# Kernel tuning notes

Hardware: AMD Instinct MI355X
Metric: run time of the kernel (lower is better)

The kernel has to match this reference:

```python
import jax, jax.numpy as jnp
import numpy as np

B, EMBED, H, W = 16, 256, 64, 64
HEADS, POINTS = 8, 4  # mmcv MultiScaleDeformableAttention defaults, num_levels=1


def make_pe(d, h, w):
    # LoFTR-style PositionEncodingSine: pe[0::4]=sin(x*div), pe[1::4]=cos(x*div),
    # pe[2::4]=sin(y*div), pe[3::4]=cos(y*div); x,y are 1-based cumsum positions.
    y = jnp.broadcast_to(jnp.arange(1, h + 1, dtype=jnp.float32)[:, None], (h, w))
    x = jnp.broadcast_to(jnp.arange(1, w + 1, dtype=jnp.float32)[None, :], (h, w))
    div = jnp.exp(jnp.arange(0, d // 2, 2, dtype=jnp.float32) * (-np.log(10000.0) / (d // 2)))
    div = div[:, None, None]  # (d//4,1,1)
    pe = jnp.stack([jnp.sin(x * div), jnp.cos(x * div), jnp.sin(y * div), jnp.cos(y * div)], axis=1)
    return pe.reshape(d, h, w)[None]  # (1,d,h,w)


def reference_points(h, w):
    # Faithful to original: meshgrid(linspace(0,1,W), linspace(0,1,H), indexing='ij'),
    # stack (col, row), flatten -> (W*H, 2)
    gx, gy = jnp.meshgrid(jnp.linspace(0.0, 1.0, w), jnp.linspace(0.0, 1.0, h), indexing='ij')
    return jnp.stack([gy, gx], -1).reshape(-1, 2)


def reference(query, value, W_off, b_off, W_attn, b_attn, W_val, b_val, W_out, b_out):
    Bq, C, h, w = query.shape
    N = h * w
    d = C // HEADS
    pe = make_pe(C, h, w)
    q = query + pe  # query += self.pe(query)
    q_flat = q.reshape(Bq, C, N).transpose(0, 2, 1)      # (B,N,C)
    v_flat = value.reshape(Bq, C, N).transpose(0, 2, 1)  # (B,N,C)
    # value projection, split heads: (B,heads,N,d) -- spatial index n = y*w + x
    v = (v_flat @ W_val.T + b_val).reshape(Bq, N, HEADS, d).transpose(0, 2, 1, 3)
    off = (q_flat @ W_off.T + b_off).reshape(Bq, N, HEADS, POINTS, 2)
    attn = jax.nn.softmax((q_flat @ W_attn.T + b_attn).reshape(Bq, N, HEADS, POINTS), axis=-1)
    ref = reference_points(h, w)                          # (N,2)
    normalizer = jnp.array([w, h], jnp.float32)           # (W, H) per mmcv
    loc = ref[None, :, None, None, :] + off / normalizer  # (B,N,heads,P,2) in [0,1]
    grid = 2.0 * loc - 1.0                                # grid_sample coords, align_corners=False
    sx = grid[..., 0].transpose(0, 2, 1, 3).reshape(Bq, HEADS, N * POINTS)
    sy = grid[..., 1].transpose(0, 2, 1, 3).reshape(Bq, HEADS, N * POINTS)
    ix = (sx + 1.0) * w * 0.5 - 0.5
    iy = (sy + 1.0) * h * 0.5 - 0.5
    x0f = jnp.floor(ix); y0f = jnp.floor(iy)
    wx = ix - x0f; wy = iy - y0f
    x0 = x0f.astype(jnp.int32); y0 = y0f.astype(jnp.int32)

    def gather(yi, xi):
        # zero padding outside the image
        valid = (xi >= 0) & (xi < w) & (yi >= 0) & (yi < h)
        idx = jnp.clip(yi, 0, h - 1) * w + jnp.clip(xi, 0, w - 1)  # (B,heads,M)
        g = jnp.take_along_axis(v, idx[..., None], axis=2)          # (B,heads,M,d)
        return g * valid[..., None]

    samp = (((1 - wx) * (1 - wy))[..., None] * gather(y0, x0)
            + (wx * (1 - wy))[..., None] * gather(y0, x0 + 1)
            + ((1 - wx) * wy)[..., None] * gather(y0 + 1, x0)
            + (wx * wy)[..., None] * gather(y0 + 1, x0 + 1))        # (B,heads,N*P,d)
    samp = samp.reshape(Bq, HEADS, N, POINTS, d)
    attn_t = attn.transpose(0, 2, 1, 3)                             # (B,heads,N,P)
    out = jnp.einsum('bhnp,bhnpd->bnhd', attn_t, samp).reshape(Bq, N, C)
    out = out @ W_out.T + b_out + q_flat  # mmcv internal identity residual (dropout in eval = id)
    out = out.transpose(0, 2, 1).reshape(Bq, C, h, w)
    return out + q  # outer residual: output + query (query already has pe added)


def setup_inputs():
    key = jax.random.key(0)
    ks = jax.random.split(key, 8)
    s = 0.02
    return {
        'query': jax.random.normal(ks[0], (B, EMBED, H, W), jnp.float32),
        'value': jax.random.normal(ks[1], (B, EMBED, H, W), jnp.float32),
        'W_off': jax.random.normal(ks[2], (HEADS * POINTS * 2, EMBED), jnp.float32) * s,
        'b_off': jax.random.normal(ks[3], (HEADS * POINTS * 2,), jnp.float32) * 2.0,
        'W_attn': jax.random.normal(ks[4], (HEADS * POINTS, EMBED), jnp.float32) * s,
        'b_attn': jnp.zeros((HEADS * POINTS,), jnp.float32),
        'W_val': jax.random.normal(ks[5], (EMBED, EMBED), jnp.float32) * s,
        'b_val': jnp.zeros((EMBED,), jnp.float32),
        'W_out': jax.random.normal(ks[6], (EMBED, EMBED), jnp.float32) * s,
        'b_out': jnp.zeros((EMBED,), jnp.float32),
    }
```

## Files before the change

### kernel.cpp

```cpp
#include <hip/hip_runtime.h>
#include <hip/hip_bf16.h>

typedef __bf16 bf16;
typedef bf16 bf16x8 __attribute__((ext_vector_type(8)));
typedef bf16 bf16x4 __attribute__((ext_vector_type(4)));
typedef float f32x4 __attribute__((ext_vector_type(4)));

#define CB 16
#define CC 256
#define CH 64
#define CW 64
#define CN 4096
#define NHEADS 8
#define NPOINTS 4
#define HDIM 32
#define SNB 8

#define MFMA16(a, b, c) __builtin_amdgcn_mfma_f32_16x16x32_bf16(a, b, c, 0, 0, 0)

__device__ __forceinline__ int swzb(int row) { return ((row >> 3) & 7) << 4; }

__global__ __launch_bounds__(256) void pe_kernel(float* __restrict__ pe) {
    int idx = blockIdx.x * 256 + threadIdx.x;
    if (idx >= CC * CN) return;
    int c = idx >> 12, n = idx & (CN - 1);
    int r = n >> 6, x = n & 63;
    int i = c >> 2, t = c & 3;
    float div = __expf(-logf(10000.0f) * (float)i / 64.0f);
    float arg = ((t < 2) ? (float)(x + 1) : (float)(r + 1)) * div;
    pe[idx] = (t & 1) ? cosf(arg) : sinf(arg);
}

__global__ __launch_bounds__(256) void pack_w(const float* __restrict__ Wv,
                                              const float* __restrict__ Woff,
                                              const float* __restrict__ Wattn,
                                              const float* __restrict__ Wout,
                                              bf16* __restrict__ Wv_bf,
                                              bf16* __restrict__ W96_bf,
                                              bf16* __restrict__ Wout_bf) {
    int i = blockIdx.x * 256 + threadIdx.x;
    if (i < CC * CC) {
        Wv_bf[i] = (bf16)Wv[i];
        Wout_bf[i] = (bf16)Wout[i];
    }
    if (i < 96 * CC) {
        W96_bf[i] = (bf16)((i < 64 * CC) ? Woff[i] : Wattn[i - 64 * CC]);
    }
}

__device__ __forceinline__ void stage_rows(const bf16* __restrict__ src, bf16 (*lds)[72],
                                           int nrows, int tid) {
    for (int i = tid; i < nrows * 8; i += 256) {
        int row = i >> 3, ch = i & 7;
        uint4 v = *reinterpret_cast<const uint4*>(src + (size_t)row * CC + ch * 8);
        *reinterpret_cast<uint4*>(&lds[row][ch * 8]) = v;
    }
}

__global__ __launch_bounds__(512) void vproj_f(const float* __restrict__ value,
                                               const bf16* __restrict__ Wv,
                                               const float* __restrict__ bv,
                                               bf16* __restrict__ v_s) {
    __shared__ float F[64][132];
    __shared__ bf16 Bs[128][72];
    char* BsC = (char*)&Bs[0][0];
    int tid = threadIdx.x, lane = tid & 63, wave = tid >> 6;
    int wm = wave >> 1, wn = wave & 1, g = lane >> 4, lr = lane & 15;
    int n0 = blockIdx.x * 128, b = blockIdx.z;
    const float* vb = value + (size_t)b * CC * CN + n0;

    int c32 = tid & 31, r = tid >> 5;
    f32x4 st[4];
#pragma unroll
    for (int p = 0; p < 4; ++p) st[p] = *(const f32x4*)&vb[(size_t)(p * 16 + r) * CN + c32 * 4];
#pragma unroll
    for (int p = 0; p < 4; ++p) *(f32x4*)&F[p * 16 + r][c32 * 4] = st[p];

    f32x4 acc[4][4] = {};
    for (int k0 = 0; k0 < CC; k0 += 64) {
        __syncthreads();
        {
            int n = tid & 127, kq = tid >> 7;
            float v[16];
#pragma unroll
            for (int i = 0; i < 16; ++i) v[i] = F[kq * 16 + i][n];
#pragma unroll
            for (int j = 0; j < 2; ++j) {
                bf16x8 o;
#pragma unroll
                for (int u = 0; u < 8; ++u) o[u] = (bf16)v[j * 8 + u];
                *(bf16x8*)(BsC + n * 144 + ((kq * 32 + j * 16) ^ swzb(n))) = o;
            }
        }
        __syncthreads();
        bool more = (k0 + 64 < CC);
        if (more) {
#pragma unroll
            for (int p = 0; p < 4; ++p)
                st[p] = *(const f32x4*)&vb[(size_t)(k0 + 64 + p * 16 + r) * CN + c32 * 4];
        }
#pragma unroll
        for (int ks = 0; ks < 2; ++ks) {
            bf16x8 af[4], bfr[4];
#pragma unroll
            for (int mf = 0; mf < 4; ++mf)
                af[mf] = *(const bf16x8*)&Wv[(size_t)(wm * 64 + mf * 16 + lr) * CC + k0 + ks * 32 + g * 8];
#pragma unroll
            for (int nf = 0; nf < 4; ++nf) {
                int row = wn * 64 + nf * 16 + lr;
                bfr[nf] = *(const bf16x8*)(BsC + row * 144 + ((ks * 64 + g * 16) ^ swzb(row)));
            }
#pragma unroll
            for (int mf = 0; mf < 4; ++mf)
#pragma unroll
                for (int nf = 0; nf < 4; ++nf)
                    acc[mf][nf] = MFMA16(af[mf], bfr[nf], acc[mf][nf]);
        }
        if (more) {
#pragma unroll
            for (int p = 0; p < 4; ++p) *(f32x4*)&F[p * 16 + r][c32 * 4] = st[p];
        }
    }

    float* T = &F[0][0];
    int dn = tid >> 2, q = tid & 3;
#pragma unroll
    for (int pass = 0; pass < 4; ++pass) {
        __syncthreads();
        if (wm == pass) {
#pragma unroll
            for (int mf = 0; mf < 4; ++mf)
#pragma unroll
                for (int nf = 0; nf < 4; ++nf)
#pragma unroll
                    for (int i = 0; i < 4; ++i)
                        T[(mf * 16 + g * 4 + i) * 132 + wn * 64 + nf * 16 + lr] = acc[mf][nf][i];
        }
        __syncthreads();
#pragma unroll
        for (int j = 0; j < 2; ++j) {
            int cg = pass * 64 + q * 16 + j * 8;
            int head = cg >> 5, dd0 = cg & 31;
            bf16x8 o;
#pragma unroll
            for (int u = 0; u < 8; ++u)
                o[u] = (bf16)(T[(q * 16 + j * 8 + u) * 132 + dn] + bv[cg + u]);
            *(bf16x8*)&v_s[(((size_t)b * NHEADS + head) * CN + n0 + dn) * HDIM + dd0] = o;
        }
    }
}

__global__ __launch_bounds__(256) void offattn_f(const float* __restrict__ query,
                                                 const float* __restrict__ pe,
                                                 const bf16* __restrict__ W96,
                                                 const float* __restrict__ boff,
                                                 const float* __restrict__ battn,
                                                 float* __restrict__ oa) {
    __shared__ float F[64][132];
    __shared__ bf16 Bs[128][72];
    char* BsC = (char*)&Bs[0][0];
    int tid = threadIdx.x, lane = tid & 63, wave = tid >> 6;
    int wm = wave >> 1, wn = wave & 1, g = lane >> 4, lr = lane & 15;
    int n0 = blockIdx.x * 128, b = blockIdx.z;
    const float* qb = query + (size_t)b * CC * CN + n0;
    const float* peb = pe + n0;

    int c32 = tid & 31, r = tid >> 5;
    f32x4 st[8];
#pragma unroll
    for (int p = 0; p < 8; ++p) {
        size_t off = (size_t)(p * 8 + r) * CN + c32 * 4;
        st[p] = *(const f32x4*)&qb[off] + *(const f32x4*)&peb[off];
    }
#pragma unroll
    for (int p = 0; p < 8; ++p) *(f32x4*)&F[p * 8 + r][c32 * 4] = st[p];

    f32x4 acc[3][4] = {};
    for (int k0 = 0; k0 < CC; k0 += 64) {
        __syncthreads();
        {
            int n = tid & 127, kh = tid >> 7;
            float v[32];
#pragma unroll
            for (int i = 0; i < 32; ++i) v[i] = F[kh * 32 + i][n];
#pragma unroll
            for (int j = 0; j < 4; ++j) {
                bf16x8 o;
#pragma unroll
                for (int u = 0; u < 8; ++u) o[u] = (bf16)v[j * 8 + u];
                *(bf16x8*)(BsC + n * 144 + ((kh * 64 + j * 16) ^ swzb(n))) = o;
            }
        }
        __syncthreads();
        bool more = (k0 + 64 < CC);
        if (more) {
#pragma unroll
            for (int p = 0; p < 8; ++p) {
                size_t off = (size_t)(k0 + 64 + p * 8 + r) * CN + c32 * 4;
                st[p] = *(const f32x4*)&qb[off] + *(const f32x4*)&peb[off];
            }
        }
#pragma unroll
        for (int ks = 0; ks < 2; ++ks) {
            bf16x8 af[3], bfr[4];
#pragma unroll
            for (int mf = 0; mf < 3; ++mf)
                af[mf] = *(const bf16x8*)&W96[(size_t)(wm * 48 + mf * 16 + lr) * CC + k0 + ks * 32 + g * 8];
#pragma unroll
            for (int nf = 0; nf < 4; ++nf) {
                int row = wn * 64 + nf * 16 + lr;
                bfr[nf] = *(const bf16x8*)(BsC + row * 144 + ((ks * 64 + g * 16) ^ swzb(row)));
            }
#pragma unroll
            for (int mf = 0; mf < 3; ++mf)
#pragma unroll
                for (int nf = 0; nf < 4; ++nf)
                    acc[mf][nf] = MFMA16(af[mf], bfr[nf], acc[mf][nf]);
        }
        if (more) {
#pragma unroll
            for (int p = 0; p < 8; ++p) *(f32x4*)&F[p * 8 + r][c32 * 4] = st[p];
        }
    }
#pragma unroll
    for (int mf = 0; mf < 3; ++mf) {
        int j0 = wm * 48 + mf * 16 + g * 4;
#pragma unroll
        for (int i = 0; i < 4; ++i) {
            int j = j0 + i;
            float bias = (j < 64) ? boff[j] : battn[j - 64];
#pragma unroll
            for (int nf = 0; nf < 4; ++nf) {
                int n = n0 + wn * 64 + nf * 16 + lr;
                oa[((size_t)b * 96 + j) * CN + n] = acc[mf][nf][i] + bias;
            }
        }
    }
}

__global__ __launch_bounds__(256) void sample_kernel(const float* __restrict__ oa,
                                                     const bf16* __restrict__ v_s,
                                                     bf16* __restrict__ s) {
    __shared__ int   lidx[SNB][NHEADS][NPOINTS][4];
    __shared__ float lwgt[SNB][NHEADS][NPOINTS][4];
    int bn0 = blockIdx.x * SNB;
    int b = bn0 >> 12;
    int tid = threadIdx.x;
    const float* ob = oa + (size_t)b * 96 * CN;

    {
        int nl = tid >> 5, head = (tid >> 2) & 7, p = tid & 3;
        int bn = bn0 + nl;
        int n = bn & (CN - 1);
        float lg0 = ob[(size_t)(64 + head * 4 + 0) * CN + n];
        float lg1 = ob[(size_t)(64 + head * 4 + 1) * CN + n];
        float lg2 = ob[(size_t)(64 + head * 4 + 2) * CN + n];
        float lg3 = ob[(size_t)(64 + head * 4 + 3) * CN + n];
        float m = fmaxf(fmaxf(lg0, lg1), fmaxf(lg2, lg3));
        float e0 = __expf(lg0 - m), e1 = __expf(lg1 - m);
        float e2 = __expf(lg2 - m), e3 = __expf(lg3 - m);
        float ep = (p == 0) ? e0 : (p == 1) ? e1 : (p == 2) ? e2 : e3;
        float a = ep / (e0 + e1 + e2 + e3);

        float off0 = ob[(size_t)(head * 8 + p * 2 + 0) * CN + n];
        float off1 = ob[(size_t)(head * 8 + p * 2 + 1) * CN + n];
        float ix = (float)(n & 63) * (64.0f / 63.0f) + off0 - 0.5f;
        float iy = (float)(n >> 6) * (64.0f / 63.0f) + off1 - 0.5f;
        float x0f = floorf(ix), y0f = floorf(iy);
        float wx = ix - x0f, wy = iy - y0f;
        int x0 = (int)x0f, y0 = (int)y0f;
        int x1 = x0 + 1, y1 = y0 + 1;
        float vx0 = (x0 >= 0 && x0 < CW) ? 1.f : 0.f;
        float vx1 = (x1 >= 0 && x1 < CW) ? 1.f : 0.f;
        float vy0 = (y0 >= 0 && y0 < CH) ? 1.f : 0.f;
        float vy1 = (y1 >= 0 && y1 < CH) ? 1.f : 0.f;
        int x0c = min(max(x0, 0), CW - 1), x1c = min(max(x1, 0), CW - 1);
        int y0c = min(max(y0, 0), CH - 1), y1c = min(max(y1, 0), CH - 1);
        lwgt[nl][head][p][0] = a * (1.f - wx) * (1.f - wy) * vx0 * vy0;
        lwgt[nl][head][p][1] = a * wx * (1.f - wy) * vx1 * vy0;
        lwgt[nl][head][p][2] = a * (1.f - wx) * wy * vx0 * vy1;
        lwgt[nl][head][p][3] = a * wx * wy * vx1 * vy1;
        lidx[nl][head][p][0] = (y0c * CW + x0c) * HDIM;
        lidx[nl][head][p][1] = (y0c * CW + x1c) * HDIM;
        lidx[nl][head][p][2] = (y1c * CW + x0c) * HDIM;
        lidx[nl][head][p][3] = (y1c * CW + x1c) * HDIM;
    }
    __syncthreads();

    int nl = tid >> 5, head = (tid >> 2) & 7, q = tid & 3;
    int bn = bn0 + nl;
    const bf16* vb = v_s + (((size_t)b * NHEADS + head) * CN) * HDIM + q * 8;
    float acc0 = 0.f, acc1 = 0.f, acc2 = 0.f, acc3 = 0.f;
    float acc4 = 0.f, acc5 = 0.f, acc6 = 0.f, acc7 = 0.f;
#pragma unroll
    for (int p = 0; p < NPOINTS; ++p) {
#pragma unroll
        for (int c = 0; c < 4; ++c) {
            float w = lwgt[nl][head][p][c];
            int id = lidx[nl][head][p][c];
            bf16x8 v = *(const bf16x8*)&vb[id];
            acc0 += w * (float)v[0];
            acc1 += w * (float)v[1];
            acc2 += w * (float)v[2];
            acc3 += w * (float)v[3];
            acc4 += w * (float)v[4];
            acc5 += w * (float)v[5];
            acc6 += w * (float)v[6];
            acc7 += w * (float)v[7];
        }
    }
    bf16x8 o;
    o[0] = (bf16)acc0; o[1] = (bf16)acc1; o[2] = (bf16)acc2; o[3] = (bf16)acc3;
    o[4] = (bf16)acc4; o[5] = (bf16)acc5; o[6] = (bf16)acc6; o[7] = (bf16)acc7;
    *(bf16x8*)&s[(size_t)bn * CC + head * HDIM + q * 8] = o;
}

__global__ __launch_bounds__(256) void outproj_mfma(const bf16* __restrict__ s_t,
                                                    const bf16* __restrict__ Wout,
                                                    const float* __restrict__ bout,
                                                    const float* __restrict__ query,
                                                    const float* __restrict__ pe,
                                                    float* __restrict__ out) {
    __shared__ __align__(16) char smem[36864];
    bf16 (*As)[72] = (bf16(*)[72])smem;
    bf16 (*Bs)[72] = (bf16(*)[72])(smem + 128 * 72 * 2);
    float* T = (float*)smem;
    const int TP = 132;

    int tid = threadIdx.x, lane = tid & 63, wave = tid >> 6;
    int wm = wave >> 1, wn = wave & 1, g = lane >> 4, lr = lane & 15;
    int n0 = blockIdx.x * 128, c0 = blockIdx.y * 128, b = blockIdx.z;
    const bf16* sb = s_t + (size_t)b * CN * CC;
    f32x4 acc[4][4] = {};
    for (int k0 = 0; k0 < CC; k0 += 64) {
        stage_rows(sb + (size_t)n0 * CC + k0, As, 128, tid);
        stage_rows(Wout + (size_t)c0 * CC + k0, Bs, 128, tid);
        __syncthreads();
#pragma unroll
        for (int ks = 0; ks < 2; ++ks) {
            bf16x8 af[4], bfr[4];
#pragma unroll
            for (int mf = 0; mf < 4; ++mf)
                af[mf] = *(const bf16x8*)&As[wm * 64 + mf * 16 + lr][ks * 32 + g * 8];
#pragma unroll
            for (int nf = 0; nf < 4; ++nf)
                bfr[nf] = *(const bf16x8*)&Bs[wn * 64 + nf * 16 + lr][ks * 32 + g * 8];
#pragma unroll
            for (int mf = 0; mf < 4; ++mf)
#pragma unroll
                for (int nf = 0; nf < 4; ++nf)
                    acc[mf][nf] = MFMA16(af[mf], bfr[nf], acc[mf][nf]);
        }
        __syncthreads();
    }

    int lr5 = tid & 31, rq = tid >> 5;
#pragma unroll
    for (int ch = 0; ch < 2; ++ch) {
        if (wn == ch) {
#pragma unroll
            for (int mf = 0; mf < 4; ++mf)
#pragma unroll
                for (int nf = 0; nf < 4; ++nf) {
                    int cl = nf * 16 + lr;
                    int nl = wm * 64 + mf * 16 + g * 4;
                    *(f32x4*)&T[cl * TP + nl] = acc[mf][nf];
                }
        }
        __syncthreads();
#pragma unroll
        for (int pass = 0; pass < 8; ++pass) {
            int cl = pass * 8 + rq;
            int c = c0 + ch * 64 + cl;
            int n = n0 + lr5 * 4;
            f32x4 v = *(const f32x4*)&T[cl * TP + lr5 * 4];
            size_t base = ((size_t)b * CC + c) * CN + n;
            f32x4 q4 = *(const f32x4*)&query[base];
            f32x4 p4 = *(const f32x4*)&pe[(size_t)c * CN + n];
            float bias = bout[c];
#pragma unroll
            for (int j = 0; j < 4; ++j) v[j] = v[j] + bias + 2.0f * (q4[j] + p4[j]);
            *(f32x4*)&out[base] = v;
        }
        __syncthreads();
    }
}

extern "C" void kernel_launch(void* const* d_in, const int* in_sizes, int n_in,
                              void* d_out, int out_size, void* d_ws, size_t ws_size,
                              hipStream_t stream) {
    const float* query = (const float*)d_in[0];
    const float* value = (const float*)d_in[1];
    const float* W_off = (const float*)d_in[2];
    const float* b_off = (const float*)d_in[3];
    const float* W_attn = (const float*)d_in[4];
    const float* b_attn = (const float*)d_in[5];
    const float* W_val = (const float*)d_in[6];
    const float* b_val = (const float*)d_in[7];
    const float* W_out = (const float*)d_in[8];
    const float* b_out = (const float*)d_in[9];
    float* out = (float*)d_out;

    char* p = (char*)d_ws;
    float* pe = (float*)p;            p += (size_t)CC * CN * 4;
    bf16* Wv_bf = (bf16*)p;           p += (size_t)CC * CC * 2;
    bf16* Wout_bf = (bf16*)p;         p += (size_t)CC * CC * 2;
    bf16* W96_bf = (bf16*)p;          p += (size_t)96 * CC * 2 + 256;
    bf16* v_s = (bf16*)p;             p += (size_t)CB * NHEADS * CN * HDIM * 2;
    float* oa = (float*)p;            p += (size_t)CB * 96 * CN * 4;
    bf16* s_t = (bf16*)p;             p += (size_t)CB * CN * CC * 2;

    pe_kernel<<<dim3((CC * CN + 255) / 256), dim3(256), 0, stream>>>(pe);
    pack_w<<<dim3(256), dim3(256), 0, stream>>>(W_val, W_off, W_attn, W_out,
                                                Wv_bf, W96_bf, Wout_bf);
    vproj_f<<<dim3(CN / 128, 1, CB), dim3(512), 0, stream>>>(value, Wv_bf, b_val, v_s);
    offattn_f<<<dim3(CN / 128, 1, CB), dim3(256), 0, stream>>>(query, pe, W96_bf,
                                                               b_off, b_attn, oa);
    sample_kernel<<<dim3(CB * CN / SNB), dim3(256), 0, stream>>>(oa, v_s, s_t);
    outproj_mfma<<<dim3(CN / 128, CC / 128, CB), dim3(256), 0, stream>>>(s_t, Wout_bf, b_out,
                                                                         query, pe, out);
}
```

Before: 167.1 us.

## Shrink projection tiles and double-buffer LDS staging; read weights directly from global

The value and offset/attention projection kernels now use 64-column tiles, which doubles the grid. Each thread loads scalar columns and converts them to bf16 straight into a swizzled LDS buffer that alternates between two slots, replacing the fp32 staging tile and its transpose pass. The output projection prefetches the next A tile into registers while computing on a double-buffered LDS tile, and it reads Wout fragments directly from global memory instead of staging them. This aims to raise occupancy and overlap global loads with MFMA work, at the cost of scalar strided global loads and more global traffic for weight fragments.

```diff
diff --git a/kernel.cpp b/kernel.cpp
--- a/kernel.cpp
+++ b/kernel.cpp
@@ -17,8 +17,6 @@
 #define SNB 8
 
 #define MFMA16(a, b, c) __builtin_amdgcn_mfma_f32_16x16x32_bf16(a, b, c, 0, 0, 0)
-
-__device__ __forceinline__ int swzb(int row) { return ((row >> 3) & 7) << 4; }
 
 __global__ __launch_bounds__(256) void pe_kernel(float* __restrict__ pe) {
     int idx = blockIdx.x * 256 + threadIdx.x;
@@ -48,82 +46,55 @@
     }
 }
 
-__device__ __forceinline__ void stage_rows(const bf16* __restrict__ src, bf16 (*lds)[72],
-                                           int nrows, int tid) {
-    for (int i = tid; i < nrows * 8; i += 256) {
-        int row = i >> 3, ch = i & 7;
-        uint4 v = *reinterpret_cast<const uint4*>(src + (size_t)row * CC + ch * 8);
-        *reinterpret_cast<uint4*>(&lds[row][ch * 8]) = v;
-    }
-}
-
 __global__ __launch_bounds__(512) void vproj_f(const float* __restrict__ value,
                                                const bf16* __restrict__ Wv,
                                                const float* __restrict__ bv,
                                                bf16* __restrict__ v_s) {
-    __shared__ float F[64][132];
-    __shared__ bf16 Bs[128][72];
-    char* BsC = (char*)&Bs[0][0];
+    __shared__ __align__(16) char smem[17408];
+    float* T = (float*)smem;
+    const int TP = 66;
+
     int tid = threadIdx.x, lane = tid & 63, wave = tid >> 6;
     int wm = wave >> 1, wn = wave & 1, g = lane >> 4, lr = lane & 15;
-    int n0 = blockIdx.x * 128, b = blockIdx.z;
-    const float* vb = value + (size_t)b * CC * CN + n0;
-
-    int c32 = tid & 31, r = tid >> 5;
-    f32x4 st[4];
-#pragma unroll
-    for (int p = 0; p < 4; ++p) st[p] = *(const f32x4*)&vb[(size_t)(p * 16 + r) * CN + c32 * 4];
-#pragma unroll
-    for (int p = 0; p < 4; ++p) *(f32x4*)&F[p * 16 + r][c32 * 4] = st[p];
-
-    f32x4 acc[4][4] = {};
-    for (int k0 = 0; k0 < CC; k0 += 64) {
-        __syncthreads();
-        {
-            int n = tid & 127, kq = tid >> 7;
-            float v[16];
-#pragma unroll
-            for (int i = 0; i < 16; ++i) v[i] = F[kq * 16 + i][n];
-#pragma unroll
-            for (int j = 0; j < 2; ++j) {
-                bf16x8 o;
-#pragma unroll
-                for (int u = 0; u < 8; ++u) o[u] = (bf16)v[j * 8 + u];
-                *(bf16x8*)(BsC + n * 144 + ((kq * 32 + j * 16) ^ swzb(n))) = o;
-            }
-        }
-        __syncthreads();
-        bool more = (k0 + 64 < CC);
-        if (more) {
-#pragma unroll
-            for (int p = 0; p < 4; ++p)
-                st[p] = *(const f32x4*)&vb[(size_t)(k0 + 64 + p * 16 + r) * CN + c32 * 4];
+    int n0 = blockIdx.x * 64, b = blockIdx.z;
+    int nl = tid & 63, kg = tid >> 6;
+    const float* src = value + (size_t)b * CC * CN + n0 + nl;
+
+    float v[8];
+#pragma unroll
+    for (int p = 0; p < 8; ++p) v[p] = src[(size_t)(kg * 8 + p) * CN];
+
+    f32x4 acc[4][2] = {};
+    for (int t = 0; t < 4; ++t) {
+        bf16x8 o;
+#pragma unroll
+        for (int p = 0; p < 8; ++p) o[p] = (bf16)v[p];
+        *(bf16x8*)(smem + (t & 1) * 8192 + nl * 128 + ((kg ^ (nl & 7)) * 16)) = o;
+        __syncthreads();
+        if (t < 3) {
+#pragma unroll
+            for (int p = 0; p < 8; ++p) v[p] = src[(size_t)((t + 1) * 64 + kg * 8 + p) * CN];
         }
 #pragma unroll
         for (int ks = 0; ks < 2; ++ks) {
-            bf16x8 af[4], bfr[4];
-#pragma unroll
-            for (int mf = 0; mf < 4; ++mf)
-                af[mf] = *(const bf16x8*)&Wv[(size_t)(wm * 64 + mf * 16 + lr) * CC + k0 + ks * 32 + g * 8];
-#pragma unroll
-            for (int nf = 0; nf < 4; ++nf) {
-                int row = wn * 64 + nf * 16 + lr;
-                bfr[nf] = *(const bf16x8*)(BsC + row * 144 + ((ks * 64 + g * 16) ^ swzb(row)));
-            }
-#pragma unroll
-            for (int mf = 0; mf < 4; ++mf)
-#pragma unroll
-                for (int nf = 0; nf < 4; ++nf)
+            bf16x8 af[4], bfr[2];
+#pragma unroll
+            for (int mf = 0; mf < 4; ++mf)
+                af[mf] = *(const bf16x8*)&Wv[(size_t)(wm * 64 + mf * 16 + lr) * CC + t * 64 + ks * 32 + g * 8];
+#pragma unroll
+            for (int nf = 0; nf < 2; ++nf) {
+                int row = wn * 32 + nf * 16 + lr;
+                bfr[nf] = *(const bf16x8*)(smem + (t & 1) * 8192 + row * 128 + (((ks * 4 + g) ^ (row & 7)) * 16));
+            }
+#pragma unroll
+            for (int mf = 0; mf < 4; ++mf)
+#pragma unroll
+                for (int nf = 0; nf < 2; ++nf)
                     acc[mf][nf] = MFMA16(af[mf], bfr[nf], acc[mf][nf]);
         }
-        if (more) {
-#pragma unroll
-            for (int p = 0; p < 4; ++p) *(f32x4*)&F[p * 16 + r][c32 * 4] = st[p];
-        }
-    }
-
-    float* T = &F[0][0];
-    int dn = tid >> 2, q = tid & 3;
+    }
+
+    int q = tid & 3, n_l = (tid >> 2) & 63, hh = tid >> 8;
 #pragma unroll
     for (int pass = 0; pass < 4; ++pass) {
         __syncthreads();
@@ -131,22 +102,18 @@
 #pragma unroll
             for (int mf = 0; mf < 4; ++mf)
 #pragma unroll
-                for (int nf = 0; nf < 4; ++nf)
+                for (int nf = 0; nf < 2; ++nf)
 #pragma unroll
                     for (int i = 0; i < 4; ++i)
-                        T[(mf * 16 + g * 4 + i) * 132 + wn * 64 + nf * 16 + lr] = acc[mf][nf][i];
-        }
-        __syncthreads();
-#pragma unroll
-        for (int j = 0; j < 2; ++j) {
-            int cg = pass * 64 + q * 16 + j * 8;
-            int head = cg >> 5, dd0 = cg & 31;
-            bf16x8 o;
-#pragma unroll
-            for (int u = 0; u < 8; ++u)
-                o[u] = (bf16)(T[(q * 16 + j * 8 + u) * 132 + dn] + bv[cg + u]);
-            *(bf16x8*)&v_s[(((size_t)b * NHEADS + head) * CN + n0 + dn) * HDIM + dd0] = o;
-        }
+                        T[(mf * 16 + g * 4 + i) * TP + wn * 32 + nf * 16 + lr] = acc[mf][nf][i];
+        }
+        __syncthreads();
+        int head = pass * 2 + hh;
+        bf16x8 o;
+#pragma unroll
+        for (int u = 0; u < 8; ++u)
+            o[u] = (bf16)(T[(hh * 32 + q * 8 + u) * TP + n_l] + bv[pass * 64 + hh * 32 + q * 8 + u]);
+        *(bf16x8*)&v_s[(((size_t)b * NHEADS + head) * CN + n0 + n_l) * HDIM + q * 8] = o;
     }
 }
 
@@ -156,83 +123,67 @@
                                                  const float* __restrict__ boff,
                                                  const float* __restrict__ battn,
                                                  float* __restrict__ oa) {
-    __shared__ float F[64][132];
-    __shared__ bf16 Bs[128][72];
-    char* BsC = (char*)&Bs[0][0];
+    __shared__ __align__(16) char smem[16384];
     int tid = threadIdx.x, lane = tid & 63, wave = tid >> 6;
     int wm = wave >> 1, wn = wave & 1, g = lane >> 4, lr = lane & 15;
-    int n0 = blockIdx.x * 128, b = blockIdx.z;
-    const float* qb = query + (size_t)b * CC * CN + n0;
-    const float* peb = pe + n0;
-
-    int c32 = tid & 31, r = tid >> 5;
-    f32x4 st[8];
-#pragma unroll
-    for (int p = 0; p < 8; ++p) {
-        size_t off = (size_t)(p * 8 + r) * CN + c32 * 4;
-        st[p] = *(const f32x4*)&qb[off] + *(const f32x4*)&peb[off];
-    }
-#pragma unroll
-    for (int p = 0; p < 8; ++p) *(f32x4*)&F[p * 8 + r][c32 * 4] = st[p];
-
-    f32x4 acc[3][4] = {};
-    for (int k0 = 0; k0 < CC; k0 += 64) {
-        __syncthreads();
-        {
-            int n = tid & 127, kh = tid >> 7;
-            float v[32];
-#pragma unroll
-            for (int i = 0; i < 32; ++i) v[i] = F[kh * 32 + i][n];
-#pragma unroll
-            for (int j = 0; j < 4; ++j) {
-                bf16x8 o;
-#pragma unroll
-                for (int u = 0; u < 8; ++u) o[u] = (bf16)v[j * 8 + u];
-                *(bf16x8*)(BsC + n * 144 + ((kh * 64 + j * 16) ^ swzb(n))) = o;
-            }
-        }
-        __syncthreads();
-        bool more = (k0 + 64 < CC);
-        if (more) {
-#pragma unroll
-            for (int p = 0; p < 8; ++p) {
-                size_t off = (size_t)(k0 + 64 + p * 8 + r) * CN + c32 * 4;
-                st[p] = *(const f32x4*)&qb[off] + *(const f32x4*)&peb[off];
+    int n0 = blockIdx.x * 64, b = blockIdx.z;
+    int nl = tid & 63, kg = tid >> 6;
+    const float* qs = query + (size_t)b * CC * CN + n0 + nl;
+    const float* ps = pe + n0 + nl;
+
+    float v[16];
+#pragma unroll
+    for (int p = 0; p < 16; ++p) {
+        size_t off = (size_t)(kg * 16 + p) * CN;
+        v[p] = qs[off] + ps[off];
+    }
+
+    f32x4 acc[3][2] = {};
+    for (int t = 0; t < 4; ++t) {
+#pragma unroll
+        for (int half = 0; half < 2; ++half) {
+            bf16x8 o;
+#pragma unroll
+            for (int p = 0; p < 8; ++p) o[p] = (bf16)v[half * 8 + p];
+            int slot = (kg * 2 + half) ^ (nl & 7);
+            *(bf16x8*)(smem + (t & 1) * 8192 + nl * 128 + slot * 16) = o;
+        }
+        __syncthreads();
+        if (t < 3) {
+#pragma unroll
+            for (int p = 0; p < 16; ++p) {
+                size_t off = (size_t)((t + 1) * 64 + kg * 16 + p) * CN;
+                v[p] = qs[off] + ps[off];
             }
         }
 #pragma unroll
         for (int ks = 0; ks < 2; ++ks) {
-            bf16x8 af[3], bfr[4];
+            bf16x8 af[3], bfr[2];
 #pragma unroll
             for (int mf = 0; mf < 3; ++mf)
-                af[mf] = *(const bf16x8*)&W96[(size_t)(wm * 48 + mf * 16 + lr) * CC + k0 + ks * 32 + g * 8];
-#pragma unroll
-            for (int nf = 0; nf < 4; ++nf) {
-                int row = wn * 64 + nf * 16 + lr;
-                bfr[nf] = *(const bf16x8*)(BsC + row * 144 + ((ks * 64 + g * 16) ^ swzb(row)));
+                af[mf] = *(const bf16x8*)&W96[(size_t)(wm * 48 + mf * 16 + lr) * CC + t * 64 + ks * 32 + g * 8];
+#pragma unroll
+            for (int nf = 0; nf < 2; ++nf) {
+                int row = wn * 32 + nf * 16 + lr;
+                bfr[nf] = *(const bf16x8*)(smem + (t & 1) * 8192 + row * 128 + (((ks * 4 + g) ^ (row & 7)) * 16));
             }
 #pragma unroll
             for (int mf = 0; mf < 3; ++mf)
 #pragma unroll
-                for (int nf = 0; nf < 4; ++nf)
+                for (int nf = 0; nf < 2; ++nf)
                     acc[mf][nf] = MFMA16(af[mf], bfr[nf], acc[mf][nf]);
         }
-        if (more) {
-#pragma unroll
-            for (int p = 0; p < 8; ++p) *(f32x4*)&F[p * 8 + r][c32 * 4] = st[p];
-        }
     }
 #pragma unroll
     for (int mf = 0; mf < 3; ++mf) {
-        int j0 = wm * 48 + mf * 16 + g * 4;
 #pragma unroll
         for (int i = 0; i < 4; ++i) {
-            int j = j0 + i;
+            int j = wm * 48 + mf * 16 + g * 4 + i;
             float bias = (j < 64) ? boff[j] : battn[j - 64];
 #pragma unroll
-            for (int nf = 0; nf < 4; ++nf) {
-                int n = n0 + wn * 64 + nf * 16 + lr;
-                oa[((size_t)b * 96 + j) * CN + n] = acc[mf][nf][i] + bias;
+            for (int nf = 0; nf < 2; ++nf) {
+                int n = wn * 32 + nf * 16 + lr;
+                oa[((size_t)b * 96 + j) * CN + n0 + n] = acc[mf][nf][i] + bias;
             }
         }
     }
@@ -322,8 +273,6 @@
                                                     const float* __restrict__ pe,
                                                     float* __restrict__ out) {
     __shared__ __align__(16) char smem[36864];
-    bf16 (*As)[72] = (bf16(*)[72])smem;
-    bf16 (*Bs)[72] = (bf16(*)[72])(smem + 128 * 72 * 2);
     float* T = (float*)smem;
     const int TP = 132;
 
@@ -331,20 +280,38 @@
     int wm = wave >> 1, wn = wave & 1, g = lane >> 4, lr = lane & 15;
     int n0 = blockIdx.x * 128, c0 = blockIdx.y * 128, b = blockIdx.z;
     const bf16* sb = s_t + (size_t)b * CN * CC;
+
+    uint4 st[4];
+#pragma unroll
+    for (int j = 0; j < 4; ++j) {
+        int i = tid + j * 256, row = i >> 3, ch = i & 7;
+        st[j] = *(const uint4*)&sb[(size_t)(n0 + row) * CC + ch * 8];
+    }
+
     f32x4 acc[4][4] = {};
-    for (int k0 = 0; k0 < CC; k0 += 64) {
-        stage_rows(sb + (size_t)n0 * CC + k0, As, 128, tid);
-        stage_rows(Wout + (size_t)c0 * CC + k0, Bs, 128, tid);
-        __syncthreads();
+    for (int t = 0; t < 4; ++t) {
+#pragma unroll
+        for (int j = 0; j < 4; ++j) {
+            int i = tid + j * 256, row = i >> 3, ch = i & 7;
+            *(uint4*)(smem + (t & 1) * 18432 + row * 144 + ch * 16) = st[j];
+        }
+        __syncthreads();
+        if (t < 3) {
+#pragma unroll
+            for (int j = 0; j < 4; ++j) {
+                int i = tid + j * 256, row = i >> 3, ch = i & 7;
+                st[j] = *(const uint4*)&sb[(size_t)(n0 + row) * CC + (t + 1) * 64 + ch * 8];
+            }
+        }
 #pragma unroll
         for (int ks = 0; ks < 2; ++ks) {
             bf16x8 af[4], bfr[4];
 #pragma unroll
             for (int mf = 0; mf < 4; ++mf)
-                af[mf] = *(const bf16x8*)&As[wm * 64 + mf * 16 + lr][ks * 32 + g * 8];
+                af[mf] = *(const bf16x8*)(smem + (t & 1) * 18432 + (wm * 64 + mf * 16 + lr) * 144 + ks * 64 + g * 16);
 #pragma unroll
             for (int nf = 0; nf < 4; ++nf)
-                bfr[nf] = *(const bf16x8*)&Bs[wn * 64 + nf * 16 + lr][ks * 32 + g * 8];
+                bfr[nf] = *(const bf16x8*)&Wout[(size_t)(c0 + wn * 64 + nf * 16 + lr) * CC + t * 64 + ks * 32 + g * 8];
 #pragma unroll
             for (int mf = 0; mf < 4; ++mf)
 #pragma unroll
@@ -413,9 +380,9 @@
     pe_kernel<<<dim3((CC * CN + 255) / 256), dim3(256), 0, stream>>>(pe);
     pack_w<<<dim3(256), dim3(256), 0, stream>>>(W_val, W_off, W_attn, W_out,
                                                 Wv_bf, W96_bf, Wout_bf);
-    vproj_f<<<dim3(CN / 128, 1, CB), dim3(512), 0, stream>>>(value, Wv_bf, b_val, v_s);
-    offattn_f<<<dim3(CN / 128, 1, CB), dim3(256), 0, stream>>>(query, pe, W96_bf,
-                                                               b_off, b_attn, oa);
+    vproj_f<<<dim3(CN / 64, 1, CB), dim3(512), 0, stream>>>(value, Wv_bf, b_val, v_s);
+    offattn_f<<<dim3(CN / 64, 1, CB), dim3(256), 0, stream>>>(query, pe, W96_bf,
+                                                              b_off, b_attn, oa);
     sample_kernel<<<dim3(CB * CN / SNB), dim3(256), 0, stream>>>(oa, v_s, s_t);
     outproj_mfma<<<dim3(CN / 128, CC / 128, CB), dim3(256), 0, stream>>>(s_t, Wout_bf, b_out,
                                                                          query, pe, out);
```

Result: slower. 179.2 us (+7.2%).
